# Performance work log

Measured on AMD Instinct MI355X. Metric: run time of the kernel, lower is better.

## Reference

```python
import jax, jax.numpy as jnp
from jax import lax
import numpy as np

RADIUS = 0.2   # ball-query radius (module init arg)
NSAMPLE = 32   # gather_size
STRIDE = 4     # npoint = ceil(N / STRIDE)


def setup_inputs() -> dict:
    key = jax.random.key(0)
    k1, k2, k3 = jax.random.split(key, 3)
    points = jax.random.uniform(k1, (4, 8192, 3), jnp.float32)      # (B,N,3) in unit cube
    features = jax.random.normal(k2, (4, 8192, 64), jnp.float32)    # (B,N,C)
    # Conv2d(in=C+3, out=128, kernel=(1, NSAMPLE), bias=False) weight
    weight = jax.random.normal(k3, (128, 67, 1, 32), jnp.float32) * 0.02
    return {"points": points, "features": features, "weight": weight}


def fps(xyz, npoint):
    """Furthest point sampling. xyz: (B,N,3) -> inds (B,npoint) int32."""
    B, N, _ = xyz.shape
    start = jnp.zeros((B,), jnp.int32)          # standard FPS starts at index 0
    dist0 = jnp.full((B, N), 1e10, xyz.dtype)

    def body(carry, _):
        dist, last = carry
        last_xyz = jnp.take_along_axis(xyz, last[:, None, None], axis=1)  # (B,1,3)
        d = jnp.sum((xyz - last_xyz) ** 2, axis=-1)                        # (B,N)
        dist = jnp.minimum(dist, d)
        nxt = jnp.argmax(dist, axis=-1).astype(jnp.int32)
        return (dist, nxt), nxt

    (_, _), rest = lax.scan(body, (dist0, start), None, length=npoint - 1)
    return jnp.concatenate([start[None, :], rest], axis=0).T  # (B,npoint)


def ball_query(xyz, new_xyz, radius, nsample):
    """For each center, first `nsample` point indices within radius, padded with
    the first valid index (pointnet2 semantics). Returns (B,npoint,nsample)."""
    N = xyz.shape[1]
    d2 = jnp.sum((new_xyz[:, :, None, :] - xyz[:, None, :, :]) ** 2, axis=-1)  # (B,npoint,N)
    cand = jnp.where(d2 < radius * radius, jnp.arange(N, dtype=jnp.int32), N)
    neg, _ = lax.top_k(-cand, nsample)   # smallest nsample indices, in order
    idx = -neg
    first = idx[..., :1]                 # center itself is always in-ball -> valid
    return jnp.where(idx == N, first, idx)


def _forward(points, features, weight):
    B, N, _ = points.shape
    npoint = (N + STRIDE - 1) // STRIDE
    inds = fps(points, npoint)                                        # (B,npoint)
    new_xyz = jnp.take_along_axis(points, inds[..., None], axis=1)    # (B,npoint,3)
    idx = ball_query(points, new_xyz, RADIUS, NSAMPLE)                # (B,npoint,nsample)

    gather = lambda v: jax.vmap(lambda a, i: a[i])(v, idx)            # (B,npoint,nsample,*)
    g_xyz = gather(points) - new_xyz[:, :, None, :]                   # relative coords
    g_feat = gather(features)
    g = jnp.concatenate([g_xyz, g_feat], axis=-1)                     # (B,npoint,nsample,3+C)

    # Conv2d with kernel (1,nsample): contract over channel + neighbor axes.
    conv = jnp.einsum("bpsc,ocs->bpo", g, weight[:, :, 0, :])         # (B,npoint,Cout)
    return new_xyz, conv


def reference(points, features, weight):
    return _forward(points, features, weight)
```

## Files before the change

### kernel.cpp

```cpp
#include <hip/hip_runtime.h>

#define BATCH   4
#define NPTS    8192
#define NPOINT  2048
#define NSAMPLE 32
#define NCH     67
#define NOUT    128
#define FPS_T   512
#define NWAVE   (FPS_T / 64)
#define KPT     (NPTS / FPS_T)
#define NBKT    64
#define NFPS    4
#define NBLK    256
#define TPT     8
#define NTICK   (BATCH * NPOINT / TPT)

#define DPP_ROW_SHR1    0x111
#define DPP_ROW_SHR2    0x112
#define DPP_ROW_SHR4    0x114
#define DPP_ROW_SHR8    0x118
#define DPP_ROW_BCAST15 0x142
#define DPP_ROW_BCAST31 0x143

#define DPP_MAX_HOP(key, ctrl)                                                 \
    {                                                                          \
        int _lo = (int)(unsigned)(key);                                        \
        int _hi = (int)(unsigned)((key) >> 32);                                \
        int _olo = __builtin_amdgcn_update_dpp(0, _lo, (ctrl), 0xF, 0xF, true);\
        int _ohi = __builtin_amdgcn_update_dpp(0, _hi, (ctrl), 0xF, 0xF, true);\
        unsigned long long _o =                                                \
            ((unsigned long long)(unsigned)_ohi << 32) | (unsigned)_olo;       \
        if (_o > (key)) (key) = _o;                                            \
    }

#define DPP_REDUCE_MAX(key)            \
    DPP_MAX_HOP(key, DPP_ROW_SHR1);    \
    DPP_MAX_HOP(key, DPP_ROW_SHR2);    \
    DPP_MAX_HOP(key, DPP_ROW_SHR4);    \
    DPP_MAX_HOP(key, DPP_ROW_SHR8);    \
    DPP_MAX_HOP(key, DPP_ROW_BCAST15); \
    DPP_MAX_HOP(key, DPP_ROW_BCAST31);

__global__ __launch_bounds__(FPS_T) void fused_kernel(
    const float* __restrict__ points, const float* __restrict__ features,
    const float* __restrict__ weight, float* __restrict__ new_xyz,
    float* __restrict__ conv_out, int* __restrict__ ctl)
{
    __shared__ __attribute__((aligned(16))) char smem[149504];
    const int t    = threadIdx.x;
    const int lane = t & 63;
    const int w    = t >> 6;
    int* prog = ctl;
    int* ticket = ctl + 32;

    if (blockIdx.x < NFPS) {
#pragma clang fp contract(off)
        const int b = blockIdx.x;
        const float* pts = points + (size_t)b * NPTS * 3;

        float2* xy = (float2*)smem;
        float2* zd = (float2*)(smem + 65536);
        unsigned short* orig16 = (unsigned short*)(smem + 131072);
        unsigned long long (*key_g)[NBKT] =
            (unsigned long long (*)[NBKT])(smem + 147456);
        int* start  = (int*)(smem + 148480);
        int* cursor = (int*)(smem + 148744);
        float (*bbr)[NWAVE] = (float (*)[NWAVE])(smem + 149000);

        float mnx = 1e30f, mny = 1e30f, mnz = 1e30f;
        float mxx = -1e30f, mxy = -1e30f, mxz = -1e30f;
        for (int k = 0; k < KPT; ++k) {
            const int i = k * FPS_T + t;
            float xx = pts[3 * i], yy = pts[3 * i + 1], zz = pts[3 * i + 2];
            mnx = fminf(mnx, xx); mxx = fmaxf(mxx, xx);
            mny = fminf(mny, yy); mxy = fmaxf(mxy, yy);
            mnz = fminf(mnz, zz); mxz = fmaxf(mxz, zz);
        }
#pragma unroll
        for (int off = 32; off >= 1; off >>= 1) {
            mnx = fminf(mnx, __shfl_down(mnx, off));
            mny = fminf(mny, __shfl_down(mny, off));
            mnz = fminf(mnz, __shfl_down(mnz, off));
            mxx = fmaxf(mxx, __shfl_down(mxx, off));
            mxy = fmaxf(mxy, __shfl_down(mxy, off));
            mxz = fmaxf(mxz, __shfl_down(mxz, off));
        }
        if (lane == 0) {
            bbr[0][w] = mnx; bbr[1][w] = mny; bbr[2][w] = mnz;
            bbr[3][w] = mxx; bbr[4][w] = mxy; bbr[5][w] = mxz;
        }
        if (t < NBKT) cursor[t] = 0;
        __syncthreads();
        mnx = bbr[0][0]; mny = bbr[1][0]; mnz = bbr[2][0];
        mxx = bbr[3][0]; mxy = bbr[4][0]; mxz = bbr[5][0];
#pragma unroll
        for (int q = 1; q < NWAVE; ++q) {
            mnx = fminf(mnx, bbr[0][q]); mny = fminf(mny, bbr[1][q]);
            mnz = fminf(mnz, bbr[2][q]); mxx = fmaxf(mxx, bbr[3][q]);
            mxy = fmaxf(mxy, bbr[4][q]); mxz = fmaxf(mxz, bbr[5][q]);
        }
        const float rx = mxx - mnx, ry = mxy - mny, rz = mxz - mnz;
        const float sclx = (rx > 0.f) ? 4.0f / rx : 0.f;
        const float scly = (ry > 0.f) ? 4.0f / ry : 0.f;
        const float sclz = (rz > 0.f) ? 4.0f / rz : 0.f;

        for (int k = 0; k < KPT; ++k) {
            const int i = k * FPS_T + t;
            float xx = pts[3 * i], yy = pts[3 * i + 1], zz = pts[3 * i + 2];
            int cxi = min(3, max(0, (int)((xx - mnx) * sclx)));
            int cyi = min(3, max(0, (int)((yy - mny) * scly)));
            int czi = min(3, max(0, (int)((zz - mnz) * sclz)));
            atomicAdd(&cursor[cxi | (cyi << 2) | (czi << 4)], 1);
        }
        __syncthreads();
        if (t == 0) {
            int acc = 0;
            for (int g = 0; g < NBKT; ++g) { start[g] = acc; acc += cursor[g]; }
            start[NBKT] = acc;
        }
        __syncthreads();
        const int vs0 = start[lane];
        const int vln = start[lane + 1] - vs0;
        if (t < NBKT) cursor[t] = start[t];
        __syncthreads();

        for (int k = 0; k < KPT; ++k) {
            const int i = k * FPS_T + t;
            float xx = pts[3 * i], yy = pts[3 * i + 1], zz = pts[3 * i + 2];
            int cxi = min(3, max(0, (int)((xx - mnx) * sclx)));
            int cyi = min(3, max(0, (int)((yy - mny) * scly)));
            int czi = min(3, max(0, (int)((zz - mnz) * sclz)));
            int slot = atomicAdd(&cursor[cxi | (cyi << 2) | (czi << 4)], 1);
            xy[slot] = make_float2(xx, yy);
            zd[slot] = make_float2(zz, 10000000000.0f);
            orig16[slot] = (unsigned short)i;
        }

        const float cwx = rx * 0.25f, cwy = ry * 0.25f, cwz = rz * 0.25f;
        const float bxl = mnx + (float)(lane & 3) * cwx,        bxh = bxl + cwx;
        const float byl = mny + (float)((lane >> 2) & 3) * cwy, byh = byl + cwy;
        const float bzl = mnz + (float)((lane >> 4) & 3) * cwz, bzh = bzl + cwz;
        const unsigned long long below = (1ull << lane) - 1ull;

        float cx = pts[0], cy = pts[1], cz = pts[2];
        if (t == 0) {
            float* o = new_xyz + (size_t)b * NPOINT * 3;
            o[0] = cx; o[1] = cy; o[2] = cz;
        }
        unsigned long long kk =
            ((unsigned long long)__float_as_uint(10000000000.0f) << 32);
        __syncthreads();

        for (int it = 1; it < NPOINT; ++it) {
            const int par = it & 1;
            float ddx = fmaxf(fmaxf(bxl - cx, cx - bxh), 0.0f);
            float ddy = fmaxf(fmaxf(byl - cy, cy - byh), 0.0f);
            float ddz = fmaxf(fmaxf(bzl - cz, cz - bzh), 0.0f);
            float dmin2 = ddx * ddx + ddy * ddy + ddz * ddz;
            float ub = __uint_as_float((unsigned)(kk >> 32));
            bool scan = dmin2 < ub * 1.0001f + 1e-5f;
            unsigned long long m = __ballot(scan);

            const int rank = (int)__popcll(m & below);
            const bool mine = scan && ((rank & (NWAVE - 1)) == w);
            unsigned long long mw = __ballot(mine);

            while (mw) {
                const int g = __ffsll((long long)mw) - 1;
                mw &= mw - 1;
                const int s0 = __builtin_amdgcn_readlane(vs0, g);
                const int ln = __builtin_amdgcn_readlane(vln, g);
                unsigned long long bk = 0;
                for (int jo = lane; jo < ln; jo += 64) {
                    const int j = s0 + jo;
                    float2 vxy = xy[j];
                    float2 vzd = zd[j];
                    float dx = vxy.x - cx;
                    float dy = vxy.y - cy;
                    float dz = vzd.x - cz;
                    float d  = ((dx * dx) + (dy * dy)) + (dz * dz);
                    float nd = fminf(vzd.y, d);
                    zd[j].y = nd;
                    unsigned long long kkey =
                        ((unsigned long long)__float_as_uint(nd) << 32)
                      | ((unsigned)(8191 - (int)orig16[j]) << 13)
                      | (unsigned)j;
                    if (kkey > bk) bk = kkey;
                }
                DPP_REDUCE_MAX(bk);
                if (lane == 63) key_g[par][g] = bk;
            }
            __syncthreads();

            if (scan) kk = key_g[par][lane];
            unsigned long long rr = kk;
            DPP_REDUCE_MAX(rr);
            const unsigned rlo =
                (unsigned)__builtin_amdgcn_readlane((int)(unsigned)rr, 63);
            const int slot = (int)(rlo & 0x1FFFu);
            float2 wxy = xy[slot];
            float2 wzd = zd[slot];
            cx = wxy.x; cy = wxy.y; cz = wzd.x;
            if (t == 0) {
                float* o = new_xyz + ((size_t)b * NPOINT + it) * 3;
                o[0] = cx; o[1] = cy; o[2] = cz;
                if (((it & 15) == 15) || (it == NPOINT - 1)) {
                    __threadfence();
                    __hip_atomic_store(&prog[b], it + 1, __ATOMIC_RELEASE,
                                       __HIP_MEMORY_SCOPE_AGENT);
                }
            }
        }
        return;
    }

    float (*g)[NCH][NSAMPLE] = (float (*)[NCH][NSAMPLE])smem;
    int (*idx)[NSAMPLE] = (int (*)[NSAMPLE])(smem + 68608);
    int* tk_s = (int*)(smem + 69632);

    for (;;) {
        if (t == 0) *tk_s = atomicAdd(ticket, 1);
        __syncthreads();
        const int T = *tk_s;
        __syncthreads();
        if (T >= NTICK) break;
        const int b   = T & 3;
        const int it0 = (T >> 2) * TPT;

        if (t == 0) {
            while (__hip_atomic_load(&prog[b], __ATOMIC_ACQUIRE,
                                     __HIP_MEMORY_SCOPE_AGENT) < it0 + TPT)
                __builtin_amdgcn_s_sleep(8);
        }
        __syncthreads();

        const float* pts = points + (size_t)b * NPTS * 3;
        const float* fts = features + (size_t)b * NPTS * 64;

        {
#pragma clang fp contract(off)
            const int gci = b * NPOINT + it0 + w;
            const float cx = new_xyz[3 * gci + 0];
            const float cy = new_xyz[3 * gci + 1];
            const float cz = new_xyz[3 * gci + 2];
            const float r2 = (float)(0.2 * 0.2);
            int* out = idx[w];
            int cnt = 0, first = 0;
            bool havefirst = false;
            for (int base = 0; base < NPTS && cnt < NSAMPLE; base += 64) {
                const int j = base + lane;
                float dx = pts[3 * j + 0] - cx;
                float dy = pts[3 * j + 1] - cy;
                float dz = pts[3 * j + 2] - cz;
                float d2 = ((dx * dx) + (dy * dy)) + (dz * dz);
                const bool in = d2 < r2;
                unsigned long long m = __ballot(in);
                if (in) {
                    int pos = cnt + __popcll(m & ((1ull << lane) - 1ull));
                    if (pos < NSAMPLE) out[pos] = j;
                }
                if (!havefirst && m != 0ull) {
                    first = base + (__ffsll((long long)m) - 1);
                    havefirst = true;
                }
                cnt += __popcll(m);
            }
            if (lane >= cnt && lane < NSAMPLE) out[lane] = first;
        }
        __syncthreads();

        if (t < TPT * NSAMPLE) {
            const int p = t >> 5;
            const int s = t & 31;
            const int gci = b * NPOINT + it0 + p;
            const int j = idx[p][s];
            const float* pj = pts + 3 * j;
            g[p][0][s] = pj[0] - new_xyz[3 * gci + 0];
            g[p][1][s] = pj[1] - new_xyz[3 * gci + 1];
            g[p][2][s] = pj[2] - new_xyz[3 * gci + 2];
            const float4* fj = (const float4*)(fts + (size_t)j * 64);
#pragma unroll
            for (int c4 = 0; c4 < 16; ++c4) {
                float4 v = fj[c4];
                g[p][3 + 4 * c4 + 0][s] = v.x;
                g[p][3 + 4 * c4 + 1][s] = v.y;
                g[p][3 + 4 * c4 + 2][s] = v.z;
                g[p][3 + 4 * c4 + 3][s] = v.w;
            }
        }
        __syncthreads();

        {
            const int o = t & 127;
            const int q = t >> 7;
            float acc0 = 0.f, acc1 = 0.f;
            const float* wr = weight + (size_t)o * NCH * NSAMPLE;
            for (int c = 0; c < NCH; ++c) {
                const float4* w4 = (const float4*)(wr + c * NSAMPLE);
#pragma unroll
                for (int s4 = 0; s4 < 8; ++s4) {
                    float4 wv = w4[s4];
                    float4 g0 = *(const float4*)&g[q][c][s4 * 4];
                    float4 g1 = *(const float4*)&g[q + 4][c][s4 * 4];
                    acc0 += g0.x * wv.x + g0.y * wv.y + g0.z * wv.z + g0.w * wv.w;
                    acc1 += g1.x * wv.x + g1.y * wv.y + g1.z * wv.z + g1.w * wv.w;
                }
            }
            float* outp = conv_out + ((size_t)b * NPOINT + it0) * NOUT;
            outp[(q    ) * NOUT + o] = acc0;
            outp[(q + 4) * NOUT + o] = acc1;
        }
        __syncthreads();
    }
}

extern "C" void kernel_launch(void* const* d_in, const int* in_sizes, int n_in,
                              void* d_out, int out_size, void* d_ws, size_t ws_size,
                              hipStream_t stream)
{
    const float* points   = (const float*)d_in[0];
    const float* features = (const float*)d_in[1];
    const float* weight   = (const float*)d_in[2];

    float* new_xyz = (float*)d_out;
    float* conv    = (float*)d_out + (size_t)BATCH * NPOINT * 3;
    int* ctl = (int*)d_ws;

    hipMemsetAsync(d_ws, 0, 256, stream);
    fused_kernel<<<NBLK, FPS_T, 0, stream>>>(points, features, weight,
                                             new_xyz, conv, ctl);
}
```

Baseline: 1.999 ms.

## Replace progress-counter handoff with sentinel-filled output polling and batched center stores

The FPS blocks now stage 16 centers in shared memory and flush them with relaxed atomic stores from 48 threads, dropping the per-iteration global stores, threadfence and release counter. Consumer blocks no longer wait on a progress counter. Each wave polls its own center coordinates in new_xyz, which is pre-filled with a 0xFF sentinel by an extra memset, and the centers are cached in shared memory. This removes fence and acquire overhead on the FPS critical path. In exchange it adds a memset and relies on relaxed per-word visibility with a sentinel value that a real coordinate cannot take.

New measurement: 1.848 ms. 7.5% less time.

```diff
diff --git a/kernel.cpp b/kernel.cpp
--- a/kernel.cpp
+++ b/kernel.cpp
@@ -14,6 +14,7 @@
 #define NBLK    256
 #define TPT     8
 #define NTICK   (BATCH * NPOINT / TPT)
+#define SENT    0xFFFFFFFFu
 
 #define DPP_ROW_SHR1    0x111
 #define DPP_ROW_SHR2    0x112
@@ -50,13 +51,13 @@
     const int t    = threadIdx.x;
     const int lane = t & 63;
     const int w    = t >> 6;
-    int* prog = ctl;
-    int* ticket = ctl + 32;
+    int* ticket = ctl;
 
     if (blockIdx.x < NFPS) {
 #pragma clang fp contract(off)
         const int b = blockIdx.x;
         const float* pts = points + (size_t)b * NPTS * 3;
+        int* nxz_i = (int*)(new_xyz + (size_t)b * NPOINT * 3);
 
         float2* xy = (float2*)smem;
         float2* zd = (float2*)(smem + 65536);
@@ -66,6 +67,7 @@
         int* start  = (int*)(smem + 148480);
         int* cursor = (int*)(smem + 148744);
         float (*bbr)[NWAVE] = (float (*)[NWAVE])(smem + 149000);
+        float* cbuf = (float*)(smem + 149192);
 
         float mnx = 1e30f, mny = 1e30f, mnz = 1e30f;
         float mxx = -1e30f, mxy = -1e30f, mxz = -1e30f;
@@ -143,10 +145,7 @@
         const unsigned long long below = (1ull << lane) - 1ull;
 
         float cx = pts[0], cy = pts[1], cz = pts[2];
-        if (t == 0) {
-            float* o = new_xyz + (size_t)b * NPOINT * 3;
-            o[0] = cx; o[1] = cy; o[2] = cz;
-        }
+        if (t == 0) { cbuf[0] = cx; cbuf[1] = cy; cbuf[2] = cz; }
         unsigned long long kk =
             ((unsigned long long)__float_as_uint(10000000000.0f) << 32);
         __syncthreads();
@@ -202,13 +201,14 @@
             float2 wzd = zd[slot];
             cx = wxy.x; cy = wxy.y; cz = wzd.x;
             if (t == 0) {
-                float* o = new_xyz + ((size_t)b * NPOINT + it) * 3;
-                o[0] = cx; o[1] = cy; o[2] = cz;
-                if (((it & 15) == 15) || (it == NPOINT - 1)) {
-                    __threadfence();
-                    __hip_atomic_store(&prog[b], it + 1, __ATOMIC_RELEASE,
-                                       __HIP_MEMORY_SCOPE_AGENT);
-                }
+                const int rs = (it & 15) * 3;
+                cbuf[rs] = cx; cbuf[rs + 1] = cy; cbuf[rs + 2] = cz;
+            }
+            if (((it & 15) == 15) && t < 48) {
+                const int base3 = (it & ~15) * 3;
+                __hip_atomic_store(&nxz_i[base3 + t],
+                                   __float_as_int(cbuf[t]),
+                                   __ATOMIC_RELAXED, __HIP_MEMORY_SCOPE_AGENT);
             }
         }
         return;
@@ -216,7 +216,10 @@
 
     float (*g)[NCH][NSAMPLE] = (float (*)[NCH][NSAMPLE])smem;
     int (*idx)[NSAMPLE] = (int (*)[NSAMPLE])(smem + 68608);
-    int* tk_s = (int*)(smem + 69632);
+    float (*cc)[4] = (float (*)[4])(smem + 69632);
+    int* tk_s = (int*)(smem + 69760);
+
+    const int* nxz_all = (const int*)new_xyz;
 
     for (;;) {
         if (t == 0) *tk_s = atomicAdd(ticket, 1);
@@ -227,31 +230,49 @@
         const int b   = T & 3;
         const int it0 = (T >> 2) * TPT;
 
-        if (t == 0) {
-            while (__hip_atomic_load(&prog[b], __ATOMIC_ACQUIRE,
-                                     __HIP_MEMORY_SCOPE_AGENT) < it0 + TPT)
-                __builtin_amdgcn_s_sleep(8);
-        }
-        __syncthreads();
-
         const float* pts = points + (size_t)b * NPTS * 3;
         const float* fts = features + (size_t)b * NPTS * 64;
+        const int gci = b * NPOINT + it0 + w;
+
+        float cxw = 0.f, cyw = 0.f, czw = 0.f;
+        if (lane == 0) {
+            unsigned v;
+            do {
+                v = (unsigned)__hip_atomic_load(&nxz_all[3 * gci + 0],
+                        __ATOMIC_RELAXED, __HIP_MEMORY_SCOPE_AGENT);
+                if (v != SENT) break;
+                __builtin_amdgcn_s_sleep(2);
+            } while (true);
+            cxw = __uint_as_float(v);
+            do {
+                v = (unsigned)__hip_atomic_load(&nxz_all[3 * gci + 1],
+                        __ATOMIC_RELAXED, __HIP_MEMORY_SCOPE_AGENT);
+                if (v != SENT) break;
+                __builtin_amdgcn_s_sleep(2);
+            } while (true);
+            cyw = __uint_as_float(v);
+            do {
+                v = (unsigned)__hip_atomic_load(&nxz_all[3 * gci + 2],
+                        __ATOMIC_RELAXED, __HIP_MEMORY_SCOPE_AGENT);
+                if (v != SENT) break;
+                __builtin_amdgcn_s_sleep(2);
+            } while (true);
+            czw = __uint_as_float(v);
+        }
+        cxw = __shfl(cxw, 0); cyw = __shfl(cyw, 0); czw = __shfl(czw, 0);
+        if (lane == 0) { cc[w][0] = cxw; cc[w][1] = cyw; cc[w][2] = czw; }
 
         {
 #pragma clang fp contract(off)
-            const int gci = b * NPOINT + it0 + w;
-            const float cx = new_xyz[3 * gci + 0];
-            const float cy = new_xyz[3 * gci + 1];
-            const float cz = new_xyz[3 * gci + 2];
             const float r2 = (float)(0.2 * 0.2);
             int* out = idx[w];
             int cnt = 0, first = 0;
             bool havefirst = false;
             for (int base = 0; base < NPTS && cnt < NSAMPLE; base += 64) {
                 const int j = base + lane;
-                float dx = pts[3 * j + 0] - cx;
-                float dy = pts[3 * j + 1] - cy;
-                float dz = pts[3 * j + 2] - cz;
+                float dx = pts[3 * j + 0] - cxw;
+                float dy = pts[3 * j + 1] - cyw;
+                float dz = pts[3 * j + 2] - czw;
                 float d2 = ((dx * dx) + (dy * dy)) + (dz * dz);
                 const bool in = d2 < r2;
                 unsigned long long m = __ballot(in);
@@ -272,12 +293,11 @@
         if (t < TPT * NSAMPLE) {
             const int p = t >> 5;
             const int s = t & 31;
-            const int gci = b * NPOINT + it0 + p;
             const int j = idx[p][s];
             const float* pj = pts + 3 * j;
-            g[p][0][s] = pj[0] - new_xyz[3 * gci + 0];
-            g[p][1][s] = pj[1] - new_xyz[3 * gci + 1];
-            g[p][2][s] = pj[2] - new_xyz[3 * gci + 2];
+            g[p][0][s] = pj[0] - cc[p][0];
+            g[p][1][s] = pj[1] - cc[p][1];
+            g[p][2][s] = pj[2] - cc[p][2];
             const float4* fj = (const float4*)(fts + (size_t)j * 64);
 #pragma unroll
             for (int c4 = 0; c4 < 16; ++c4) {
@@ -326,7 +346,8 @@
     float* conv    = (float*)d_out + (size_t)BATCH * NPOINT * 3;
     int* ctl = (int*)d_ws;
 
-    hipMemsetAsync(d_ws, 0, 256, stream);
+    hipMemsetAsync(d_ws, 0, 64, stream);
+    hipMemsetAsync(new_xyz, 0xFF, (size_t)BATCH * NPOINT * 3 * 4, stream);
     fused_kernel<<<NBLK, FPS_T, 0, stream>>>(points, features, weight,
                                              new_xyz, conv, ctl);
 }
```
